# Kernel optimization log

Hardware: AMD Instinct MI355X
Metric: run time of the kernel (lower is better)

Reference implementation:

```python
import jax, jax.numpy as jnp
import numpy as np

T, B, IN, H, OUT = 2048, 512, 27, 64, 26
EPS = 1e-5
DROP = 0.1


def setup_inputs() -> dict:
    key = jax.random.key(0)
    ks = jax.random.split(key, 11)
    s = 1.0 / np.sqrt(H)
    u = lambda k, shape: jax.random.uniform(k, shape, jnp.float32, -s, s)
    return {
        "obscure_word": jax.random.normal(ks[0], (T, B, IN), jnp.float32),
        "prev_guess": jax.random.uniform(ks[1], (T, OUT), jnp.float32),
        "W_ih": u(ks[2], (4 * H, IN)),
        "W_hh": u(ks[3], (4 * H, H)),
        "b_ih": u(ks[4], (4 * H,)),
        "b_hh": u(ks[5], (4 * H,)),
        "gamma": jnp.ones((H,), jnp.float32),
        "beta": jnp.zeros((H,), jnp.float32),
        "W_fc": u(ks[6], (OUT, H + OUT)),
        "b_fc": u(ks[7], (OUT,)),
        # LockedDropout mask: sampled once, reused every timestep, pre-scaled by 1/(1-p)
        "drop_mask": (jax.random.uniform(ks[8], (B, H)) < (1.0 - DROP)).astype(jnp.float32) / (1.0 - DROP),
    }


def reference(obscure_word, prev_guess, W_ih, W_hh, b_ih, b_hh, gamma, beta, W_fc, b_fc, drop_mask):
    h0 = jnp.zeros((B, H), obscure_word.dtype)
    c0 = jnp.zeros((B, H), obscure_word.dtype)

    def step(carry, inputs):
        h, c = carry
        x_t, pg_t = inputs  # [B, IN], [OUT]
        gates = x_t @ W_ih.T + b_ih + h @ W_hh.T + b_hh  # [B, 4H]
        i, f, g, o = jnp.split(gates, 4, axis=1)
        i = jax.nn.sigmoid(i)
        f = jax.nn.sigmoid(f)
        g = jnp.tanh(g)
        o = jax.nn.sigmoid(o)
        c_new = f * c + i * g
        h_new = o * jnp.tanh(c_new)
        # BatchNorm1d (training mode: per-timestep batch stats, biased var)
        mean = jnp.mean(h_new, axis=0)
        var = jnp.mean((h_new - mean) ** 2, axis=0)
        hb = (h_new - mean) * jax.lax.rsqrt(var + EPS) * gamma + beta
        # LockedDropout (same mask every timestep)
        hd = hb * drop_mask
        # MaxPool1d over batch dim -> [H]
        pooled = jnp.max(hd, axis=0)
        out = jnp.concatenate([pooled, pg_t])  # [H+OUT]
        y = out @ W_fc.T + b_fc  # [OUT]
        return (h_new, c_new), y

    _, ys = jax.lax.scan(step, (h0, c0), (obscure_word, prev_guess))
    return ys[:, None, :]  # [T, 1, OUT]
```

## Files before the change

kernel.cpp:

```cpp
#include <hip/hip_runtime.h>

#define TT   2048
#define BB   512
#define IN_  27
#define HH   64
#define OUTD 26
#define EPSV 1e-5f

__device__ __forceinline__ float bcastf(float v, int lane) {
    return __int_as_float(__builtin_amdgcn_readlane(__float_as_int(v), lane));
}

__device__ __forceinline__ float sigm(float x) {
    return 1.0f / (1.0f + __expf(-x));
}

__device__ __forceinline__ float tanh_fast(float x) {
    float e = __expf(-2.0f * fabsf(x));
    float r = (1.0f - e) / (1.0f + e);
    return copysignf(r, x);
}

__global__ void __launch_bounds__(256)
__attribute__((amdgpu_waves_per_eu(2, 2)))
lstm_seq(
    const float* __restrict__ x,
    const float* __restrict__ W_ih,
    const float* __restrict__ W_hh,
    const float* __restrict__ b_ih,
    const float* __restrict__ b_hh,
    float* __restrict__ h_all,
    float* __restrict__ state,
    int t0, int tc, int first)
{
    const int b   = blockIdx.x;
    const int wid = threadIdx.x >> 6;
    const int l   = threadIdx.x & 63;
    const int j   = wid * HH + l;

    const float* Wp = W_hh + j * HH;
    float wh0 =Wp[0],  wh1 =Wp[1],  wh2 =Wp[2],  wh3 =Wp[3];
    float wh4 =Wp[4],  wh5 =Wp[5],  wh6 =Wp[6],  wh7 =Wp[7];
    float wh8 =Wp[8],  wh9 =Wp[9],  wh10=Wp[10], wh11=Wp[11];
    float wh12=Wp[12], wh13=Wp[13], wh14=Wp[14], wh15=Wp[15];
    float wh16=Wp[16], wh17=Wp[17], wh18=Wp[18], wh19=Wp[19];
    float wh20=Wp[20], wh21=Wp[21], wh22=Wp[22], wh23=Wp[23];
    float wh24=Wp[24], wh25=Wp[25], wh26=Wp[26], wh27=Wp[27];
    float wh28=Wp[28], wh29=Wp[29], wh30=Wp[30], wh31=Wp[31];
    float wh32=Wp[32], wh33=Wp[33], wh34=Wp[34], wh35=Wp[35];
    float wh36=Wp[36], wh37=Wp[37], wh38=Wp[38], wh39=Wp[39];
    float wh40=Wp[40], wh41=Wp[41], wh42=Wp[42], wh43=Wp[43];
    float wh44=Wp[44], wh45=Wp[45], wh46=Wp[46], wh47=Wp[47];
    float wh48=Wp[48], wh49=Wp[49], wh50=Wp[50], wh51=Wp[51];
    float wh52=Wp[52], wh53=Wp[53], wh54=Wp[54], wh55=Wp[55];
    float wh56=Wp[56], wh57=Wp[57], wh58=Wp[58], wh59=Wp[59];
    float wh60=Wp[60], wh61=Wp[61], wh62=Wp[62], wh63=Wp[63];

    const float* Ip = W_ih + j * IN_;
    float wi0 =Ip[0],  wi1 =Ip[1],  wi2 =Ip[2],  wi3 =Ip[3];
    float wi4 =Ip[4],  wi5 =Ip[5],  wi6 =Ip[6],  wi7 =Ip[7];
    float wi8 =Ip[8],  wi9 =Ip[9],  wi10=Ip[10], wi11=Ip[11];
    float wi12=Ip[12], wi13=Ip[13], wi14=Ip[14], wi15=Ip[15];
    float wi16=Ip[16], wi17=Ip[17], wi18=Ip[18], wi19=Ip[19];
    float wi20=Ip[20], wi21=Ip[21], wi22=Ip[22], wi23=Ip[23];
    float wi24=Ip[24], wi25=Ip[25], wi26=Ip[26];

    asm volatile("" : "+v"(wh0), "+v"(wh1), "+v"(wh2), "+v"(wh3),
                      "+v"(wh4), "+v"(wh5), "+v"(wh6), "+v"(wh7),
                      "+v"(wh8), "+v"(wh9), "+v"(wh10), "+v"(wh11),
                      "+v"(wh12), "+v"(wh13), "+v"(wh14), "+v"(wh15));
    asm volatile("" : "+v"(wh16), "+v"(wh17), "+v"(wh18), "+v"(wh19),
                      "+v"(wh20), "+v"(wh21), "+v"(wh22), "+v"(wh23),
                      "+v"(wh24), "+v"(wh25), "+v"(wh26), "+v"(wh27),
                      "+v"(wh28), "+v"(wh29), "+v"(wh30), "+v"(wh31));
    asm volatile("" : "+v"(wh32), "+v"(wh33), "+v"(wh34), "+v"(wh35),
                      "+v"(wh36), "+v"(wh37), "+v"(wh38), "+v"(wh39),
                      "+v"(wh40), "+v"(wh41), "+v"(wh42), "+v"(wh43),
                      "+v"(wh44), "+v"(wh45), "+v"(wh46), "+v"(wh47));
    asm volatile("" : "+v"(wh48), "+v"(wh49), "+v"(wh50), "+v"(wh51),
                      "+v"(wh52), "+v"(wh53), "+v"(wh54), "+v"(wh55),
                      "+v"(wh56), "+v"(wh57), "+v"(wh58), "+v"(wh59),
                      "+v"(wh60), "+v"(wh61), "+v"(wh62), "+v"(wh63));
    asm volatile("" : "+v"(wi0), "+v"(wi1), "+v"(wi2), "+v"(wi3),
                      "+v"(wi4), "+v"(wi5), "+v"(wi6), "+v"(wi7),
                      "+v"(wi8), "+v"(wi9), "+v"(wi10), "+v"(wi11),
                      "+v"(wi12), "+v"(wi13), "+v"(wi14), "+v"(wi15));
    asm volatile("" : "+v"(wi16), "+v"(wi17), "+v"(wi18), "+v"(wi19),
                      "+v"(wi20), "+v"(wi21), "+v"(wi22), "+v"(wi23),
                      "+v"(wi24), "+v"(wi25), "+v"(wi26));

    const float bias = b_ih[j] + b_hh[j];

    float hv, cv;
    if (first) {
        hv = 0.0f; cv = 0.0f;
    } else {
        hv = state[b * HH + l];
        cv = state[BB * HH + b * HH + l];
    }

    __shared__ float acts[2][4][HH];

#define HD(k, acc) acc = fmaf(bcastf(hv, k), wh##k, acc);
#define XD(k, acc) acc = fmaf(bcastf(xcur, k), wi##k, acc);

    float xv = (l < IN_) ? x[((size_t)t0 * BB + b) * IN_ + l] : 0.0f;
    float xpart;
    {
        const float xcur = xv;
        float p0 = 0.0f, p1 = 0.0f, p2 = 0.0f, p3 = 0.0f;
        XD(0,p0)  XD(1,p1)  XD(2,p2)  XD(3,p3)
        XD(4,p0)  XD(5,p1)  XD(6,p2)  XD(7,p3)
        XD(8,p0)  XD(9,p1)  XD(10,p2) XD(11,p3)
        XD(12,p0) XD(13,p1) XD(14,p2) XD(15,p3)
        XD(16,p0) XD(17,p1) XD(18,p2) XD(19,p3)
        XD(20,p0) XD(21,p1) XD(22,p2) XD(23,p3)
        XD(24,p0) XD(25,p1) XD(26,p2)
        xpart = (p0 + p1) + (p2 + p3);
    }
    {
        int tn = t0 + 1; if (tn > TT - 1) tn = TT - 1;
        xv = (l < IN_) ? x[((size_t)tn * BB + b) * IN_ + l] : 0.0f;
    }

    float* hout = h_all + (size_t)b * HH + l;

#pragma unroll 1
    for (int tl = 0; tl < tc; ++tl) {
        const int t = t0 + tl;

        float a0 = bias + xpart, a1 = 0.0f, a2 = 0.0f, a3 = 0.0f;
        HD(0,a0)  HD(1,a1)  HD(2,a2)  HD(3,a3)
        HD(4,a0)  HD(5,a1)  HD(6,a2)  HD(7,a3)
        HD(8,a0)  HD(9,a1)  HD(10,a2) HD(11,a3)
        HD(12,a0) HD(13,a1) HD(14,a2) HD(15,a3)
        HD(16,a0) HD(17,a1) HD(18,a2) HD(19,a3)
        HD(20,a0) HD(21,a1) HD(22,a2) HD(23,a3)
        HD(24,a0) HD(25,a1) HD(26,a2) HD(27,a3)
        HD(28,a0) HD(29,a1) HD(30,a2) HD(31,a3)
        HD(32,a0) HD(33,a1) HD(34,a2) HD(35,a3)
        HD(36,a0) HD(37,a1) HD(38,a2) HD(39,a3)
        HD(40,a0) HD(41,a1) HD(42,a2) HD(43,a3)
        HD(44,a0) HD(45,a1) HD(46,a2) HD(47,a3)
        HD(48,a0) HD(49,a1) HD(50,a2) HD(51,a3)
        HD(52,a0) HD(53,a1) HD(54,a2) HD(55,a3)
        HD(56,a0) HD(57,a1) HD(58,a2) HD(59,a3)
        HD(60,a0) HD(61,a1) HD(62,a2) HD(63,a3)
        const float acc = (a0 + a1) + (a2 + a3);

        const float av = (wid == 2) ? tanh_fast(acc) : sigm(acc);

        acts[tl & 1][wid][l] = av;
        __syncthreads();

        const float xcur = xv;
        float p0 = 0.0f, p1 = 0.0f, p2 = 0.0f, p3 = 0.0f;
        XD(0,p0)  XD(1,p1)  XD(2,p2)  XD(3,p3)
        XD(4,p0)  XD(5,p1)  XD(6,p2)  XD(7,p3)
        XD(8,p0)  XD(9,p1)  XD(10,p2) XD(11,p3)
        XD(12,p0) XD(13,p1) XD(14,p2) XD(15,p3)
        XD(16,p0) XD(17,p1) XD(18,p2) XD(19,p3)
        XD(20,p0) XD(21,p1) XD(22,p2) XD(23,p3)
        XD(24,p0) XD(25,p1) XD(26,p2)
        int tn = t + 2; if (tn > TT - 1) tn = TT - 1;
        xv = (l < IN_) ? x[((size_t)tn * BB + b) * IN_ + l] : 0.0f;
        xpart = (p0 + p1) + (p2 + p3);

        const float gi = acts[tl & 1][0][l];
        const float gf = acts[tl & 1][1][l];
        const float gg = acts[tl & 1][2][l];
        const float go = acts[tl & 1][3][l];
        cv = fmaf(gf, cv, gi * gg);
        hv = go * tanh_fast(cv);

        if (wid == 0) {
            *hout = hv;
            hout += (size_t)BB * HH;
        }
    }

#undef HD
#undef XD

    if (wid == 0) {
        state[b * HH + l] = hv;
        state[BB * HH + b * HH + l] = cv;
    }
}

__global__ __launch_bounds__(256, 2) void bn_pool_fc(
    const float* __restrict__ h_all,
    const float* __restrict__ gamma,
    const float* __restrict__ beta,
    const float* __restrict__ dmask,
    const float* __restrict__ pg,
    const float* __restrict__ W_fc,
    const float* __restrict__ b_fc,
    float* __restrict__ y,
    int t0, int tc)
{
    const int tl = blockIdx.x;
    const int t = t0 + tl;
    const int tid = threadIdx.x;
    const int g = tid >> 6;
    const int hcol = tid & 63;
    const float* hp = h_all + (size_t)tl * BB * HH;

    __shared__ float s_a[4][HH];
    __shared__ float s_b[4][HH];
    __shared__ float s_scale[HH];
    __shared__ float s_shift[HH];
    __shared__ float s_pool[HH];

    float sum = 0.0f, sq = 0.0f;
    for (int bb = g; bb < BB; bb += 4) {
        const float v = hp[bb * HH + hcol];
        sum += v;
        sq = fmaf(v, v, sq);
    }
    s_a[g][hcol] = sum;
    s_b[g][hcol] = sq;
    __syncthreads();

    if (tid < HH) {
        const float s  = (s_a[0][tid] + s_a[1][tid]) + (s_a[2][tid] + s_a[3][tid]);
        const float q2 = (s_b[0][tid] + s_b[1][tid]) + (s_b[2][tid] + s_b[3][tid]);
        const float mean = s * (1.0f / BB);
        const float var  = q2 * (1.0f / BB) - mean * mean;
        const float rs = rsqrtf(var + EPSV);
        const float sc = rs * gamma[tid];
        s_scale[tid] = sc;
        s_shift[tid] = beta[tid] - mean * sc;
    }
    __syncthreads();

    const float sc = s_scale[hcol];
    const float sh = s_shift[hcol];
    float m = -3.0e38f;
    for (int bb = g; bb < BB; bb += 4) {
        const float v = hp[bb * HH + hcol];
        const float hd = fmaf(v, sc, sh) * dmask[bb * HH + hcol];
        m = fmaxf(m, hd);
    }
    s_a[g][hcol] = m;
    __syncthreads();
    if (tid < HH) {
        s_pool[tid] = fmaxf(fmaxf(s_a[0][tid], s_a[1][tid]),
                            fmaxf(s_a[2][tid], s_a[3][tid]));
    }
    __syncthreads();

    if (tid < OUTD) {
        float acc = b_fc[tid];
        const float* w = W_fc + tid * (HH + OUTD);
#pragma unroll
        for (int k = 0; k < HH; ++k) acc = fmaf(w[k], s_pool[k], acc);
#pragma unroll
        for (int k = 0; k < OUTD; ++k) acc = fmaf(w[HH + k], pg[t * OUTD + k], acc);
        y[t * OUTD + tid] = acc;
    }
}

extern "C" void kernel_launch(void* const* d_in, const int* in_sizes, int n_in,
                              void* d_out, int out_size, void* d_ws, size_t ws_size,
                              hipStream_t stream)
{
    const float* x     = (const float*)d_in[0];
    const float* pg    = (const float*)d_in[1];
    const float* W_ih  = (const float*)d_in[2];
    const float* W_hh  = (const float*)d_in[3];
    const float* b_ih  = (const float*)d_in[4];
    const float* b_hh  = (const float*)d_in[5];
    const float* gamma = (const float*)d_in[6];
    const float* beta  = (const float*)d_in[7];
    const float* W_fc  = (const float*)d_in[8];
    const float* b_fc  = (const float*)d_in[9];
    const float* dmask = (const float*)d_in[10];
    float* y = (float*)d_out;

    const size_t state_bytes = 2ull * BB * HH * sizeof(float);
    const size_t per_t = (size_t)BB * HH * sizeof(float);
    size_t avail = (ws_size > state_bytes) ? (ws_size - state_bytes) : 0;
    int chunkT = (int)(avail / per_t);
    if (chunkT > TT) chunkT = TT;
    if (chunkT < 1) chunkT = 1;

    float* h_all = (float*)d_ws;
    float* state = (float*)((char*)d_ws + (size_t)chunkT * per_t);

    int first = 1;
    for (int t0 = 0; t0 < TT; t0 += chunkT) {
        int tc = TT - t0;
        if (tc > chunkT) tc = chunkT;
        lstm_seq<<<BB, 256, 0, stream>>>(x, W_ih, W_hh, b_ih, b_hh,
                                         h_all, state, t0, tc, first);
        bn_pool_fc<<<tc, 256, 0, stream>>>(h_all, gamma, beta, dmask, pg,
                                           W_fc, b_fc, y, t0, tc);
        first = 0;
    }
}
```

Before: 2.335 ms.

## Hoist input projection into a separate parallel pre-GEMM kernel

Computes x_t·W_ih^T plus both biases for every timestep and batch row in a new parallel kernel before the recurrence. The sequential LSTM kernel then loads one precomputed gate value per step instead of doing 27 readlane-FMAs and holding 27 W_ih registers. The cost is a large extra workspace buffer (BB*256 floats per timestep), which shrinks chunkT and may mean more chunks. It also adds heavy global traffic to write and read the pre-gates, with one strided global load per thread per step on the critical loop.

```diff
diff --git a/kernel.cpp b/kernel.cpp
--- a/kernel.cpp
+++ b/kernel.cpp
@@ -4,6 +4,7 @@
 #define BB   512
 #define IN_  27
 #define HH   64
+#define NG   256
 #define OUTD 26
 #define EPSV 1e-5f
 
@@ -21,17 +22,47 @@
     return copysignf(r, x);
 }
 
+__global__ __launch_bounds__(256, 2) void pregemm(
+    const float* __restrict__ x,
+    const float* __restrict__ W_ih,
+    const float* __restrict__ b_ih,
+    const float* __restrict__ b_hh,
+    float* __restrict__ pre_g,
+    int t0, int tc)
+{
+    const int tl = blockIdx.x;
+    const int b0 = blockIdx.y * 8;
+    const int j  = threadIdx.x;
+
+    __shared__ float s_x[8][IN_];
+    if (j < 8 * IN_) {
+        const int bi = j / IN_, k = j % IN_;
+        s_x[bi][k] = x[(((size_t)(t0 + tl)) * BB + b0 + bi) * IN_ + k];
+    }
+
+    const float bias = b_ih[j] + b_hh[j];
+    float w[IN_];
+#pragma unroll
+    for (int k = 0; k < IN_; ++k) w[k] = W_ih[j * IN_ + k];
+    __syncthreads();
+
+#pragma unroll
+    for (int bi = 0; bi < 8; ++bi) {
+        float acc = bias;
+#pragma unroll
+        for (int k = 0; k < IN_; ++k) acc = fmaf(w[k], s_x[bi][k], acc);
+        pre_g[((size_t)tl * BB + b0 + bi) * NG + j] = acc;
+    }
+}
+
 __global__ void __launch_bounds__(256)
 __attribute__((amdgpu_waves_per_eu(2, 2)))
 lstm_seq(
-    const float* __restrict__ x,
-    const float* __restrict__ W_ih,
+    const float* __restrict__ pre_g,
     const float* __restrict__ W_hh,
-    const float* __restrict__ b_ih,
-    const float* __restrict__ b_hh,
     float* __restrict__ h_all,
     float* __restrict__ state,
-    int t0, int tc, int first)
+    int tc, int first)
 {
     const int b   = blockIdx.x;
     const int wid = threadIdx.x >> 6;
@@ -56,15 +87,6 @@
     float wh56=Wp[56], wh57=Wp[57], wh58=Wp[58], wh59=Wp[59];
     float wh60=Wp[60], wh61=Wp[61], wh62=Wp[62], wh63=Wp[63];
 
-    const float* Ip = W_ih + j * IN_;
-    float wi0 =Ip[0],  wi1 =Ip[1],  wi2 =Ip[2],  wi3 =Ip[3];
-    float wi4 =Ip[4],  wi5 =Ip[5],  wi6 =Ip[6],  wi7 =Ip[7];
-    float wi8 =Ip[8],  wi9 =Ip[9],  wi10=Ip[10], wi11=Ip[11];
-    float wi12=Ip[12], wi13=Ip[13], wi14=Ip[14], wi15=Ip[15];
-    float wi16=Ip[16], wi17=Ip[17], wi18=Ip[18], wi19=Ip[19];
-    float wi20=Ip[20], wi21=Ip[21], wi22=Ip[22], wi23=Ip[23];
-    float wi24=Ip[24], wi25=Ip[25], wi26=Ip[26];
-
     asm volatile("" : "+v"(wh0), "+v"(wh1), "+v"(wh2), "+v"(wh3),
                       "+v"(wh4), "+v"(wh5), "+v"(wh6), "+v"(wh7),
                       "+v"(wh8), "+v"(wh9), "+v"(wh10), "+v"(wh11),
@@ -81,15 +103,6 @@
                       "+v"(wh52), "+v"(wh53), "+v"(wh54), "+v"(wh55),
                       "+v"(wh56), "+v"(wh57), "+v"(wh58), "+v"(wh59),
                       "+v"(wh60), "+v"(wh61), "+v"(wh62), "+v"(wh63));
-    asm volatile("" : "+v"(wi0), "+v"(wi1), "+v"(wi2), "+v"(wi3),
-                      "+v"(wi4), "+v"(wi5), "+v"(wi6), "+v"(wi7),
-                      "+v"(wi8), "+v"(wi9), "+v"(wi10), "+v"(wi11),
-                      "+v"(wi12), "+v"(wi13), "+v"(wi14), "+v"(wi15));
-    asm volatile("" : "+v"(wi16), "+v"(wi17), "+v"(wi18), "+v"(wi19),
-                      "+v"(wi20), "+v"(wi21), "+v"(wi22), "+v"(wi23),
-                      "+v"(wi24), "+v"(wi25), "+v"(wi26));
-
-    const float bias = b_ih[j] + b_hh[j];
 
     float hv, cv;
     if (first) {
@@ -102,34 +115,18 @@
     __shared__ float acts[2][4][HH];
 
 #define HD(k, acc) acc = fmaf(bcastf(hv, k), wh##k, acc);
-#define XD(k, acc) acc = fmaf(bcastf(xcur, k), wi##k, acc);
-
-    float xv = (l < IN_) ? x[((size_t)t0 * BB + b) * IN_ + l] : 0.0f;
-    float xpart;
-    {
-        const float xcur = xv;
-        float p0 = 0.0f, p1 = 0.0f, p2 = 0.0f, p3 = 0.0f;
-        XD(0,p0)  XD(1,p1)  XD(2,p2)  XD(3,p3)
-        XD(4,p0)  XD(5,p1)  XD(6,p2)  XD(7,p3)
-        XD(8,p0)  XD(9,p1)  XD(10,p2) XD(11,p3)
-        XD(12,p0) XD(13,p1) XD(14,p2) XD(15,p3)
-        XD(16,p0) XD(17,p1) XD(18,p2) XD(19,p3)
-        XD(20,p0) XD(21,p1) XD(22,p2) XD(23,p3)
-        XD(24,p0) XD(25,p1) XD(26,p2)
-        xpart = (p0 + p1) + (p2 + p3);
-    }
-    {
-        int tn = t0 + 1; if (tn > TT - 1) tn = TT - 1;
-        xv = (l < IN_) ? x[((size_t)tn * BB + b) * IN_ + l] : 0.0f;
-    }
+
+    const float* pgp = pre_g + (size_t)b * NG + j;
+    float pgv = pgp[0];
 
     float* hout = h_all + (size_t)b * HH + l;
 
 #pragma unroll 1
     for (int tl = 0; tl < tc; ++tl) {
-        const int t = t0 + tl;
-
-        float a0 = bias + xpart, a1 = 0.0f, a2 = 0.0f, a3 = 0.0f;
+        float a0 = pgv, a1 = 0.0f, a2 = 0.0f, a3 = 0.0f;
+        int tn = tl + 1; if (tn > tc - 1) tn = tc - 1;
+        pgv = pgp[(size_t)tn * BB * NG];
+
         HD(0,a0)  HD(1,a1)  HD(2,a2)  HD(3,a3)
         HD(4,a0)  HD(5,a1)  HD(6,a2)  HD(7,a3)
         HD(8,a0)  HD(9,a1)  HD(10,a2) HD(11,a3)
@@ -153,19 +150,6 @@
         acts[tl & 1][wid][l] = av;
         __syncthreads();
 
-        const float xcur = xv;
-        float p0 = 0.0f, p1 = 0.0f, p2 = 0.0f, p3 = 0.0f;
-        XD(0,p0)  XD(1,p1)  XD(2,p2)  XD(3,p3)
-        XD(4,p0)  XD(5,p1)  XD(6,p2)  XD(7,p3)
-        XD(8,p0)  XD(9,p1)  XD(10,p2) XD(11,p3)
-        XD(12,p0) XD(13,p1) XD(14,p2) XD(15,p3)
-        XD(16,p0) XD(17,p1) XD(18,p2) XD(19,p3)
-        XD(20,p0) XD(21,p1) XD(22,p2) XD(23,p3)
-        XD(24,p0) XD(25,p1) XD(26,p2)
-        int tn = t + 2; if (tn > TT - 1) tn = TT - 1;
-        xv = (l < IN_) ? x[((size_t)tn * BB + b) * IN_ + l] : 0.0f;
-        xpart = (p0 + p1) + (p2 + p3);
-
         const float gi = acts[tl & 1][0][l];
         const float gf = acts[tl & 1][1][l];
         const float gg = acts[tl & 1][2][l];
@@ -180,7 +164,6 @@
     }
 
 #undef HD
-#undef XD
 
     if (wid == 0) {
         state[b * HH + l] = hv;
@@ -279,21 +262,23 @@
     float* y = (float*)d_out;
 
     const size_t state_bytes = 2ull * BB * HH * sizeof(float);
-    const size_t per_t = (size_t)BB * HH * sizeof(float);
+    const size_t per_t = (size_t)BB * (HH + NG) * sizeof(float);
     size_t avail = (ws_size > state_bytes) ? (ws_size - state_bytes) : 0;
     int chunkT = (int)(avail / per_t);
     if (chunkT > TT) chunkT = TT;
     if (chunkT < 1) chunkT = 1;
 
     float* h_all = (float*)d_ws;
-    float* state = (float*)((char*)d_ws + (size_t)chunkT * per_t);
+    float* preg  = h_all + (size_t)chunkT * BB * HH;
+    float* state = preg  + (size_t)chunkT * BB * NG;
 
     int first = 1;
     for (int t0 = 0; t0 < TT; t0 += chunkT) {
         int tc = TT - t0;
         if (tc > chunkT) tc = chunkT;
-        lstm_seq<<<BB, 256, 0, stream>>>(x, W_ih, W_hh, b_ih, b_hh,
-                                         h_all, state, t0, tc, first);
+        pregemm<<<dim3(tc, BB / 8), 256, 0, stream>>>(x, W_ih, b_ih, b_hh,
+                                                      preg, t0, tc);
+        lstm_seq<<<BB, 256, 0, stream>>>(preg, W_hh, h_all, state, tc, first);
         bn_pool_fc<<<tc, 256, 0, stream>>>(h_all, gamma, beta, dmask, pg,
                                            W_fc, b_fc, y, t0, tc);
         first = 0;
```

Result: slower. 2.440 ms (+4.5%).
